# Kernel optimization log

Hardware: AMD Instinct MI355X
Metric: run time of the kernel (lower is better)

## Reference

```python
import jax, jax.numpy as jnp
import numpy as np

H, C = 4, 32            # num_heads, hidden_channels per head
HC = H * C
SLOPE_ATT = 0.2         # GATv2Conv negative_slope default
SLOPE_OUT = 0.01        # F.leaky_relu default

N_HOST, N_VM, N_JOB, N_SWITCH = 50000, 100000, 200000, 5000
IN_DIM = 64
E_HS, E_VH, E_JV = 200000, 400000, 800000


def _gatv2(x_src, x_dst, Wl, bl, Wr, br, att, bias, src, dst, n_dst):
    # PyG GATv2Conv (bipartite): lin_l on source, lin_r on destination
    xl = (x_src @ Wl + bl).reshape(-1, H, C)             # [Ns,H,C]
    xr = (x_dst @ Wr + br).reshape(-1, H, C)             # [Nd,H,C]
    e = jax.nn.leaky_relu(xl[src] + xr[dst], SLOPE_ATT)  # [E,H,C]
    logits = jnp.einsum('ehc,hc->eh', e, att)            # [E,H]
    m = jax.ops.segment_max(logits, dst, num_segments=n_dst)
    ex = jnp.exp(logits - m[dst])
    denom = jax.ops.segment_sum(ex, dst, num_segments=n_dst)
    alpha = ex / denom[dst]                              # scatter-softmax grouped by dst
    out = jax.ops.segment_sum(xl[src] * alpha[..., None], dst, num_segments=n_dst)
    return out.reshape(n_dst, HC) + bias, alpha


def setup_inputs() -> dict:
    key = jax.random.key(0)
    ks = iter(jax.random.split(key, 64))
    f32 = jnp.float32
    def randn(shape, scale=1.0):
        return jax.random.normal(next(ks), shape, dtype=f32) * scale
    sw = 1.0 / np.sqrt(IN_DIM)
    sa = 1.0 / np.sqrt(C)
    inp = {
        'x_host': randn((N_HOST, IN_DIM)),
        'x_vm': randn((N_VM, IN_DIM)),
        'x_job': randn((N_JOB, IN_DIM)),
        'x_switch': randn((N_SWITCH, IN_DIM)),
        'e_hs_src': jax.random.randint(next(ks), (E_HS,), 0, N_HOST),
        'e_hs_dst': jax.random.randint(next(ks), (E_HS,), 0, N_SWITCH),
        'e_vh_src': jax.random.randint(next(ks), (E_VH,), 0, N_VM),
        'e_vh_dst': jax.random.randint(next(ks), (E_VH,), 0, N_HOST),
        'e_jv_src': jax.random.randint(next(ks), (E_JV,), 0, N_JOB),
        'e_jv_dst': jax.random.randint(next(ks), (E_JV,), 0, N_VM),
    }
    for rel in ('hs', 'vh', 'jv'):
        inp['Wl_' + rel] = randn((IN_DIM, HC), sw)
        inp['bl_' + rel] = jnp.zeros((HC,), f32)
        inp['Wr_' + rel] = randn((IN_DIM, HC), sw)
        inp['br_' + rel] = jnp.zeros((HC,), f32)
        inp['att_' + rel] = randn((H, C), sa)
        inp['bias_' + rel] = jnp.zeros((HC,), f32)
    for nt in ('host', 'vm', 'job', 'switch'):
        inp['W_' + nt] = randn((HC, 1), 1.0 / np.sqrt(HC))
        inp['b_' + nt] = jnp.zeros((1,), f32)
    return inp


def reference(x_host, x_vm, x_job, x_switch,
              e_hs_src, e_hs_dst, e_vh_src, e_vh_dst, e_jv_src, e_jv_dst,
              Wl_hs, bl_hs, Wr_hs, br_hs, att_hs, bias_hs,
              Wl_vh, bl_vh, Wr_vh, br_vh, att_vh, bias_vh,
              Wl_jv, bl_jv, Wr_jv, br_jv, att_jv, bias_jv,
              W_host, b_host, W_vm, b_vm, W_job, b_job, W_switch, b_switch):
    out_switch, a_hs = _gatv2(x_host, x_switch, Wl_hs, bl_hs, Wr_hs, br_hs,
                              att_hs, bias_hs, e_hs_src, e_hs_dst, x_switch.shape[0])
    out_host, a_vh = _gatv2(x_vm, x_host, Wl_vh, bl_vh, Wr_vh, br_vh,
                            att_vh, bias_vh, e_vh_src, e_vh_dst, x_host.shape[0])
    out_vm, a_jv = _gatv2(x_job, x_vm, Wl_jv, bl_jv, Wr_jv, br_jv,
                          att_jv, bias_jv, e_jv_src, e_jv_dst, x_vm.shape[0])
    # each dst type receives exactly one relation; stack+sum is identity here
    h_host = jax.nn.leaky_relu(out_host, SLOPE_OUT)
    h_vm = jax.nn.leaky_relu(out_vm, SLOPE_OUT)
    h_switch = jax.nn.leaky_relu(out_switch, SLOPE_OUT)
    h_job = jnp.zeros((x_job.shape[0], HC), x_job.dtype)  # job has no incoming edges
    s_host = jax.nn.sigmoid(h_host @ W_host + b_host)
    s_vm = jax.nn.sigmoid(h_vm @ W_vm + b_vm)
    s_job = jax.nn.sigmoid(h_job @ W_job + b_job)
    s_switch = jax.nn.sigmoid(h_switch @ W_switch + b_switch)
    scores = jnp.concatenate([s_host, s_vm, s_job, s_switch], axis=0)
    return scores, a_hs, a_vh, a_jv
```

## Files before the change

kernel.cpp:

```cpp
#include <hip/hip_runtime.h>
#include <hip/hip_fp16.h>


#define SLOPE_ATT 0.2f
#define SLOPE_OUT 0.01f

typedef _Float16 half8_t __attribute__((ext_vector_type(8)));
typedef _Float16 v2h_t __attribute__((ext_vector_type(2)));
typedef float float4_t __attribute__((ext_vector_type(4)));

__device__ __forceinline__ float dot8(half8_t a, half8_t b, float acc) {
    v2h_t a0 = __builtin_shufflevector(a, a, 0, 1);
    v2h_t a1 = __builtin_shufflevector(a, a, 2, 3);
    v2h_t a2 = __builtin_shufflevector(a, a, 4, 5);
    v2h_t a3 = __builtin_shufflevector(a, a, 6, 7);
    v2h_t b0 = __builtin_shufflevector(b, b, 0, 1);
    v2h_t b1 = __builtin_shufflevector(b, b, 2, 3);
    v2h_t b2 = __builtin_shufflevector(b, b, 4, 5);
    v2h_t b3 = __builtin_shufflevector(b, b, 6, 7);
    acc = __builtin_amdgcn_fdot2(a0, b0, acc, false);
    acc = __builtin_amdgcn_fdot2(a1, b1, acc, false);
    acc = __builtin_amdgcn_fdot2(a2, b2, acc, false);
    acc = __builtin_amdgcn_fdot2(a3, b3, acc, false);
    return acc;
}

struct WSrc { const float* W[6]; };

__global__ __launch_bounds__(256) void init_wt_kernel(
    int* __restrict__ head, int ptot, WSrc wsrc, __half* __restrict__ Wt) {
    int i = blockIdx.x * 256 + threadIdx.x;
    if (i < ptot) {
        head[i] = -1;
    } else {
        int r = i - ptot;
        if (r < 6 * 8192) {
            int j = r >> 13;
            int rr = r & 8191;
            int n = rr >> 6, k = rr & 63;
            Wt[r] = (__half)wsrc.W[j][k * 128 + n];
        }
    }
}

__device__ __forceinline__ void link_work(
    int linkId, int linkBlocks,
    const int* __restrict__ d0, const int* __restrict__ s0,
    const int* __restrict__ d1, const int* __restrict__ s1,
    const int* __restrict__ d2, const int* __restrict__ s2,
    int* __restrict__ head, int2* __restrict__ nxt,
    int E0, int E1, int E2, int pb1, int pb2) {
    int i = linkId * 256 + threadIdx.x;
    int Etot = E0 + E1 + E2;
    int stride = linkBlocks * 256;
    for (; i < Etot; i += stride) {
        int le, slot; const int* sp;
        if (i < E0)           { le = i;           slot = d0[le];       sp = s0; }
        else if (i < E0 + E1) { le = i - E0;      slot = pb1 + d1[le]; sp = s1; }
        else                  { le = i - E0 - E1; slot = pb2 + d2[le]; sp = s2; }
        int old = atomicExch(&head[slot], le);
        nxt[i] = make_int2(old, sp[le]);
    }
}

struct GemmJobs {
    const float* X[6]; const float* b[6]; __half* Y[6];
    int M[6]; int pbase[7];
};

__global__ __launch_bounds__(256) void mega_gemm_link_kernel(
    GemmJobs j, const __half* __restrict__ Wt, int LB,
    const int* __restrict__ d0, const int* __restrict__ s0,
    const int* __restrict__ d1, const int* __restrict__ s1,
    const int* __restrict__ d2, const int* __restrict__ s2,
    int* __restrict__ head, int2* __restrict__ nxt,
    int E0, int E1, int E2, int pb1, int pb2) {
    __shared__ __half sY[4][16][136];
    int b = blockIdx.x;
    if (b < LB) {
        link_work(b, LB, d0, s0, d1, s1, d2, s2, head, nxt, E0, E1, E2, pb1, pb2);
        return;
    }
    int bb = b - LB;
    int k = 0;
    while (bb >= j.pbase[k + 1]) k++;
    const int p = bb - j.pbase[k];
    const int gb = j.pbase[k + 1] - j.pbase[k];
    const int M = j.M[k];
    const int nb = (M + 63) >> 6;
    if (p >= nb) return;
    const float* __restrict__ X = j.X[k];
    __half* __restrict__ Y = j.Y[k];
    const float* __restrict__ bb_ = j.b[k];
    const __half* __restrict__ W = Wt + (size_t)k * 8192;

    const int lane = threadIdx.x & 63;
    const int wv = threadIdx.x >> 6;
    const int mr = lane & 15;
    const int quad = lane >> 4;

    half8_t wb0[8], wb1[8];
    float bv[8];
#pragma unroll
    for (int t = 0; t < 8; t++) {
        const __half* wp = W + ((size_t)(t * 16 + mr)) * 64 + quad * 8;
        wb0[t] = *(const half8_t*)wp;
        wb1[t] = *(const half8_t*)(wp + 32);
        bv[t] = bb_[t * 16 + mr];
    }

    float4 xc0 = {}, xc1 = {}, xc2 = {}, xc3 = {};
    {
        int gr = p * 64 + wv * 16 + mr;
        if (gr < M) {
            const float4* xp = (const float4*)(X + (size_t)gr * 64 + quad * 8);
            xc0 = xp[0]; xc1 = xp[1];
            const float4* xq = (const float4*)(X + (size_t)gr * 64 + 32 + quad * 8);
            xc2 = xq[0]; xc3 = xq[1];
        }
    }

    for (int t = p; t < nb; t += gb) {
        int tn = t + gb;
        float4 xn0 = {}, xn1 = {}, xn2 = {}, xn3 = {};
        if (tn < nb) {
            int gr = tn * 64 + wv * 16 + mr;
            if (gr < M) {
                const float4* xp = (const float4*)(X + (size_t)gr * 64 + quad * 8);
                xn0 = xp[0]; xn1 = xp[1];
                const float4* xq = (const float4*)(X + (size_t)gr * 64 + 32 + quad * 8);
                xn2 = xq[0]; xn3 = xq[1];
            }
        }

        half8_t a0, a1;
        a0[0] = (_Float16)xc0.x; a0[1] = (_Float16)xc0.y;
        a0[2] = (_Float16)xc0.z; a0[3] = (_Float16)xc0.w;
        a0[4] = (_Float16)xc1.x; a0[5] = (_Float16)xc1.y;
        a0[6] = (_Float16)xc1.z; a0[7] = (_Float16)xc1.w;
        a1[0] = (_Float16)xc2.x; a1[1] = (_Float16)xc2.y;
        a1[2] = (_Float16)xc2.z; a1[3] = (_Float16)xc2.w;
        a1[4] = (_Float16)xc3.x; a1[5] = (_Float16)xc3.y;
        a1[6] = (_Float16)xc3.z; a1[7] = (_Float16)xc3.w;

        const int m0 = t * 64 + wv * 16;
#pragma unroll
        for (int tt = 0; tt < 8; tt++) {
            float4_t c = {0.f, 0.f, 0.f, 0.f};
            c = __builtin_amdgcn_mfma_f32_16x16x32_f16(a0, wb0[tt], c, 0, 0, 0);
            c = __builtin_amdgcn_mfma_f32_16x16x32_f16(a1, wb1[tt], c, 0, 0, 0);
            int ocol = tt * 16 + mr;
            int lrow = quad * 4;
#pragma unroll
            for (int r = 0; r < 4; r++)
                sY[wv][lrow + r][ocol] = (__half)(c[r] + bv[tt]);
        }

        const int c8 = mr * 8;
#pragma unroll
        for (int i = 0; i < 4; i++) {
            int row = i * 4 + quad;
            int gr2 = m0 + row;
            if (gr2 < M) {
                half8_t v = *(const half8_t*)&sY[wv][row][c8];
                *(half8_t*)&Y[(size_t)gr2 * 128 + c8] = v;
            }
        }

        xc0 = xn0; xc1 = xn1; xc2 = xn2; xc3 = xn3;
    }
}

struct AggJob {
    const __half* xl; const __half* xr; const float* att;
    const int* head; const int2* nxt;
    float* ex; float* dn;
    const float* bias; const float* Wn; const float* bn; float* scores;
    int Nd;
};
struct AggJobs { AggJob r[3]; int base[4]; };

__global__ __launch_bounds__(256) void agg3_kernel(AggJobs aj) {
    int b = blockIdx.x;
    int k = 0;
    while (b >= aj.base[k + 1]) k++;
    AggJob J = aj.r[k];

    const int l = threadIdx.x & 63;
    const int wv = threadIdx.x >> 6;
    const int li = l & 7;
    const int g = l >> 3;
    const int dbase = ((b - aj.base[k]) * 4 + wv) * 8;
    const int d = dbase + g;
    if (dbase >= J.Nd) return;
    const bool dok = d < J.Nd;
    const int h = li >> 1;

    half8_t xr0 = {}, xr1 = {};
    if (dok) {
        const half8_t* xrp = (const half8_t*)(J.xr + (size_t)d * 128) + li * 2;
        xr0 = xrp[0]; xr1 = xrp[1];
    }
    half8_t at0, at1;
    {
        const float* ap = J.att + li * 16;
#pragma unroll
        for (int i = 0; i < 8; i++) {
            at0[i] = (_Float16)ap[i];
            at1[i] = (_Float16)ap[8 + i];
        }
    }
    const half8_t sl8 = {(_Float16)SLOPE_ATT, (_Float16)SLOPE_ATT,
                         (_Float16)SLOPE_ATT, (_Float16)SLOPE_ATT,
                         (_Float16)SLOPE_ATT, (_Float16)SLOPE_ATT,
                         (_Float16)SLOPE_ATT, (_Float16)SLOPE_ATT};

    float acc[16] = {};
    float ssum = 0.f;

    int e = dok ? J.head[d] : -1;
    const bool any = (e >= 0);

    while (__any(e >= 0)) {
        bool act = (e >= 0);
        int2 ns = act ? J.nxt[e] : make_int2(-1, 0);
        half8_t x0 = {}, x1 = {};
        if (act) {
            const half8_t* xp = (const half8_t*)(J.xl + (size_t)ns.y * 128) + li * 2;
            x0 = xp[0]; x1 = xp[1];
        }
        if (act) {
            half8_t v0 = x0 + xr0;
            half8_t v1 = x1 + xr1;
            half8_t lk0 = __builtin_elementwise_max(v0, v0 * sl8);
            half8_t lk1 = __builtin_elementwise_max(v1, v1 * sl8);
            float p = dot8(lk1, at1, dot8(lk0, at0, 0.f));
            p += __shfl_xor(p, 1);
            float w = __expf(p);
            if ((li & 1) == 0) J.ex[(size_t)e * 4 + h] = w;
            ssum += w;
#pragma unroll
            for (int i = 0; i < 8; i++) {
                acc[i]     += w * (float)x0[i];
                acc[8 + i] += w * (float)x1[i];
            }
        }
        e = act ? ns.x : -1;
    }

    if (dok && (li & 1) == 0) J.dn[(size_t)d * 4 + h] = ssum;

    float rr = any ? 1.f / ssum : 0.f;
    float pr = 0.f;
    if (dok) {
        const float* bp = J.bias + li * 16;
        const float* wp = J.Wn + li * 16;
#pragma unroll
        for (int i = 0; i < 16; i++) {
            float o = acc[i] * rr + bp[i];
            o = o > 0.f ? o : SLOPE_OUT * o;
            pr += o * wp[i];
        }
    }
    pr += __shfl_xor(pr, 1);
    pr += __shfl_xor(pr, 2);
    pr += __shfl_xor(pr, 4);
    if (dok && li == 0)
        J.scores[d] = 1.f / (1.f + __expf(-(pr + J.bn[0])));
}

__global__ __launch_bounds__(256) void alpha_job_kernel(
    float* __restrict__ ex,
    const int* __restrict__ d0, const int* __restrict__ d1,
    const int* __restrict__ d2,
    const float* __restrict__ dn,
    int E0, int E1, int E2, int pb1, int pb2, int ab,
    const float* __restrict__ bjob, float* __restrict__ sjob, int NJ) {
    int b = blockIdx.x;
    if (b < ab) {
        int i = b * 256 + threadIdx.x;
        int tot = (E0 + E1 + E2) * 4;
        if (i >= tot) return;
        int e = i >> 2, h = i & 3;
        int d;
        if (e < E0)           d = d0[e];
        else if (e < E0 + E1) d = pb1 + d1[e - E0];
        else                  d = pb2 + d2[e - E0 - E1];
        ex[i] = ex[i] / dn[(size_t)d * 4 + h];
    } else {
        int i = (b - ab) * 256 + threadIdx.x;
        if (i < NJ) sjob[i] = 1.f / (1.f + __expf(-bjob[0]));
    }
}


extern "C" void kernel_launch(void* const* d_in, const int* in_sizes, int n_in,
                              void* d_out, int out_size, void* d_ws, size_t ws_size,
                              hipStream_t stream) {
    const float* x_host   = (const float*)d_in[0];
    const float* x_vm     = (const float*)d_in[1];
    const float* x_job    = (const float*)d_in[2];
    const float* x_switch = (const float*)d_in[3];
    const int* e_hs_src = (const int*)d_in[4];
    const int* e_hs_dst = (const int*)d_in[5];
    const int* e_vh_src = (const int*)d_in[6];
    const int* e_vh_dst = (const int*)d_in[7];
    const int* e_jv_src = (const int*)d_in[8];
    const int* e_jv_dst = (const int*)d_in[9];
    const float* Wl_hs = (const float*)d_in[10];
    const float* bl_hs = (const float*)d_in[11];
    const float* Wr_hs = (const float*)d_in[12];
    const float* br_hs = (const float*)d_in[13];
    const float* att_hs = (const float*)d_in[14];
    const float* bias_hs = (const float*)d_in[15];
    const float* Wl_vh = (const float*)d_in[16];
    const float* bl_vh = (const float*)d_in[17];
    const float* Wr_vh = (const float*)d_in[18];
    const float* br_vh = (const float*)d_in[19];
    const float* att_vh = (const float*)d_in[20];
    const float* bias_vh = (const float*)d_in[21];
    const float* Wl_jv = (const float*)d_in[22];
    const float* bl_jv = (const float*)d_in[23];
    const float* Wr_jv = (const float*)d_in[24];
    const float* br_jv = (const float*)d_in[25];
    const float* att_jv = (const float*)d_in[26];
    const float* bias_jv = (const float*)d_in[27];
    const float* W_host   = (const float*)d_in[28];
    const float* b_host   = (const float*)d_in[29];
    const float* W_vm     = (const float*)d_in[30];
    const float* b_vm     = (const float*)d_in[31];
    const float* W_job    = (const float*)d_in[32];
    const float* b_job    = (const float*)d_in[33];
    const float* W_switch = (const float*)d_in[34];
    const float* b_switch = (const float*)d_in[35];

    const int NH  = in_sizes[0] / 64;
    const int NV  = in_sizes[1] / 64;
    const int NJ  = in_sizes[2] / 64;
    const int NSW = in_sizes[3] / 64;
    const int EHS = in_sizes[4];
    const int EVH = in_sizes[6];
    const int EJV = in_sizes[8];
    const int Etot = EHS + EVH + EJV;

    float* out = (float*)d_out;
    float* s_host = out;
    float* s_vm = out + NH;
    float* s_job = out + NH + NV;
    float* s_sw = out + NH + NV + NJ;
    float* a_hs = out + NH + NV + NJ + NSW;
    float* a_vh = a_hs + (size_t)EHS * 4;
    float* a_jv = a_vh + (size_t)EVH * 4;

    const int pb1 = ((NSW + 255) / 256) * 256;
    const int pb2 = pb1 + ((NH + 255) / 256) * 256;
    const int ptot = pb2 + ((NV + 255) / 256) * 256;

    float* ws = (float*)d_ws;
    int2* nxt_all = (int2*)ws;
    int* head_all = (int*)(nxt_all + Etot);
    float* dn_all = (float*)(head_all + ptot);
    __half* Wt    = (__half*)(dn_all + (size_t)ptot * 4);
    __half* mats  = Wt + 6 * 8192;
    __half* xl_hs = mats;
    __half* xr_hs = xl_hs + (size_t)NH * 128;
    __half* xl_vh = xr_hs + (size_t)NSW * 128;
    __half* xr_vh = xl_vh + (size_t)NV * 128;
    __half* xl_jv = xr_vh + (size_t)NH * 128;
    __half* xr_jv = xl_jv + (size_t)NJ * 128;

    {
        WSrc w;
        w.W[0] = Wl_hs; w.W[1] = Wr_hs; w.W[2] = Wl_vh;
        w.W[3] = Wr_vh; w.W[4] = Wl_jv; w.W[5] = Wr_jv;
        int tot = ptot + 6 * 8192;
        init_wt_kernel<<<(tot + 255) / 256, 256, 0, stream>>>(head_all, ptot, w, Wt);
    }

    {
        GemmJobs j;
        const float* Xs[6] = {x_host, x_switch, x_vm, x_host, x_job, x_vm};
        const float* bs[6] = {bl_hs, br_hs, bl_vh, br_vh, bl_jv, br_jv};
        __half* Ys[6] = {xl_hs, xr_hs, xl_vh, xr_vh, xl_jv, xr_jv};
        int Ms[6] = {NH, NSW, NV, NH, NJ, NV};
        int nbk[6]; long long total_nb = 0;
        for (int k = 0; k < 6; k++) { nbk[k] = (Ms[k] + 63) / 64; total_nb += nbk[k]; }
        const int GBTOT = 1664;
        const int LB = 384;
        int pb = 0;
        for (int k = 0; k < 6; k++) {
            j.X[k] = Xs[k]; j.b[k] = bs[k]; j.Y[k] = Ys[k]; j.M[k] = Ms[k];
            j.pbase[k] = pb;
            int gb = (int)(((long long)GBTOT * nbk[k]) / total_nb);
            if (gb < 1) gb = 1;
            pb += gb;
        }
        j.pbase[6] = pb;
        mega_gemm_link_kernel<<<LB + pb, 256, 0, stream>>>(
            j, Wt, LB, e_hs_dst, e_hs_src, e_vh_dst, e_vh_src,
            e_jv_dst, e_jv_src, head_all, nxt_all, EHS, EVH, EJV, pb1, pb2);
    }

    {
        AggJobs aj;
        aj.r[0] = {xl_hs, xr_hs, att_hs, head_all + 0, nxt_all + 0,
                   a_hs, dn_all + 0,
                   bias_hs, W_switch, b_switch, s_sw, NSW};
        aj.r[1] = {xl_vh, xr_vh, att_vh, head_all + pb1, nxt_all + EHS,
                   a_vh, dn_all + (size_t)pb1 * 4,
                   bias_vh, W_host, b_host, s_host, NH};
        aj.r[2] = {xl_jv, xr_jv, att_jv, head_all + pb2, nxt_all + (EHS + EVH),
                   a_jv, dn_all + (size_t)pb2 * 4,
                   bias_jv, W_vm, b_vm, s_vm, NV};
        aj.base[0] = 0;
        aj.base[1] = (NSW + 31) / 32;
        aj.base[2] = aj.base[1] + (NH + 31) / 32;
        aj.base[3] = aj.base[2] + (NV + 31) / 32;
        agg3_kernel<<<aj.base[3], 256, 0, stream>>>(aj);
    }

    {
        int ab = (Etot * 4 + 255) / 256;
        int jb = (NJ + 255) / 256;
        alpha_job_kernel<<<ab + jb, 256, 0, stream>>>(
            a_hs, e_hs_dst, e_vh_dst, e_jv_dst, dn_all,
            EHS, EVH, EJV, pb1, pb2, ab, b_job, s_job, NJ);
    }
}
```

Before: 367.5 us.

## Fuse alpha normalization into aggregation kernel via second linked-list walk

Drops the separate alpha_job_kernel. After computing the softmax denominator, each destination group walks its edge linked list again and rescales the stored exp values in place, so the dn buffer and the gather of dst indices go away. The job-score sigmoid fill moves into the init kernel, and the aggregation kernel shrinks to 128-thread blocks to get more, smaller blocks. This costs a second pointer-chasing pass over each adjacency list, whose nxt and ex accesses are dependent and likely uncached, in exchange for removing one launch and a full pass over the edges.

```diff
diff --git a/kernel.cpp b/kernel.cpp
--- a/kernel.cpp
+++ b/kernel.cpp
@@ -28,7 +28,8 @@
 struct WSrc { const float* W[6]; };
 
 __global__ __launch_bounds__(256) void init_wt_kernel(
-    int* __restrict__ head, int ptot, WSrc wsrc, __half* __restrict__ Wt) {
+    int* __restrict__ head, int ptot, WSrc wsrc, __half* __restrict__ Wt,
+    const float* __restrict__ bjob, float* __restrict__ sjob, int NJ) {
     int i = blockIdx.x * 256 + threadIdx.x;
     if (i < ptot) {
         head[i] = -1;
@@ -39,6 +40,9 @@
             int rr = r & 8191;
             int n = rr >> 6, k = rr & 63;
             Wt[r] = (__half)wsrc.W[j][k * 128 + n];
+        } else {
+            int q = r - 6 * 8192;
+            if (q < NJ) sjob[q] = 1.f / (1.f + __expf(-bjob[0]));
         }
     }
 }
@@ -174,13 +178,13 @@
 struct AggJob {
     const __half* xl; const __half* xr; const float* att;
     const int* head; const int2* nxt;
-    float* ex; float* dn;
+    float* ex;
     const float* bias; const float* Wn; const float* bn; float* scores;
     int Nd;
 };
 struct AggJobs { AggJob r[3]; int base[4]; };
 
-__global__ __launch_bounds__(256) void agg3_kernel(AggJobs aj) {
+__global__ __launch_bounds__(128) void agg3_kernel(AggJobs aj) {
     int b = blockIdx.x;
     int k = 0;
     while (b >= aj.base[k + 1]) k++;
@@ -190,7 +194,7 @@
     const int wv = threadIdx.x >> 6;
     const int li = l & 7;
     const int g = l >> 3;
-    const int dbase = ((b - aj.base[k]) * 4 + wv) * 8;
+    const int dbase = ((b - aj.base[k]) * 2 + wv) * 8;
     const int d = dbase + g;
     if (dbase >= J.Nd) return;
     const bool dok = d < J.Nd;
@@ -248,8 +252,6 @@
         e = act ? ns.x : -1;
     }
 
-    if (dok && (li & 1) == 0) J.dn[(size_t)d * 4 + h] = ssum;
-
     float rr = any ? 1.f / ssum : 0.f;
     float pr = 0.f;
     if (dok) {
@@ -267,29 +269,16 @@
     pr += __shfl_xor(pr, 4);
     if (dok && li == 0)
         J.scores[d] = 1.f / (1.f + __expf(-(pr + J.bn[0])));
-}
-
-__global__ __launch_bounds__(256) void alpha_job_kernel(
-    float* __restrict__ ex,
-    const int* __restrict__ d0, const int* __restrict__ d1,
-    const int* __restrict__ d2,
-    const float* __restrict__ dn,
-    int E0, int E1, int E2, int pb1, int pb2, int ab,
-    const float* __restrict__ bjob, float* __restrict__ sjob, int NJ) {
-    int b = blockIdx.x;
-    if (b < ab) {
-        int i = b * 256 + threadIdx.x;
-        int tot = (E0 + E1 + E2) * 4;
-        if (i >= tot) return;
-        int e = i >> 2, h = i & 3;
-        int d;
-        if (e < E0)           d = d0[e];
-        else if (e < E0 + E1) d = pb1 + d1[e - E0];
-        else                  d = pb2 + d2[e - E0 - E1];
-        ex[i] = ex[i] / dn[(size_t)d * 4 + h];
-    } else {
-        int i = (b - ab) * 256 + threadIdx.x;
-        if (i < NJ) sjob[i] = 1.f / (1.f + __expf(-bjob[0]));
+
+    int e2 = dok ? J.head[d] : -1;
+    while (__any(e2 >= 0)) {
+        bool act = (e2 >= 0);
+        int2 ns = act ? J.nxt[e2] : make_int2(-1, 0);
+        if (act && (li & 1) == 0) {
+            size_t o = (size_t)e2 * 4 + h;
+            J.ex[o] = J.ex[o] * rr;
+        }
+        e2 = act ? ns.x : -1;
     }
 }
 
@@ -373,8 +362,9 @@
         WSrc w;
         w.W[0] = Wl_hs; w.W[1] = Wr_hs; w.W[2] = Wl_vh;
         w.W[3] = Wr_vh; w.W[4] = Wl_jv; w.W[5] = Wr_jv;
-        int tot = ptot + 6 * 8192;
-        init_wt_kernel<<<(tot + 255) / 256, 256, 0, stream>>>(head_all, ptot, w, Wt);
+        int tot = ptot + 6 * 8192 + NJ;
+        init_wt_kernel<<<(tot + 255) / 256, 256, 0, stream>>>(
+            head_all, ptot, w, Wt, b_job, s_job, NJ);
     }
 
     {
@@ -404,26 +394,15 @@
     {
         AggJobs aj;
         aj.r[0] = {xl_hs, xr_hs, att_hs, head_all + 0, nxt_all + 0,
-                   a_hs, dn_all + 0,
-                   bias_hs, W_switch, b_switch, s_sw, NSW};
+                   a_hs, bias_hs, W_switch, b_switch, s_sw, NSW};
         aj.r[1] = {xl_vh, xr_vh, att_vh, head_all + pb1, nxt_all + EHS,
-                   a_vh, dn_all + (size_t)pb1 * 4,
-                   bias_vh, W_host, b_host, s_host, NH};
+                   a_vh, bias_vh, W_host, b_host, s_host, NH};
         aj.r[2] = {xl_jv, xr_jv, att_jv, head_all + pb2, nxt_all + (EHS + EVH),
-                   a_jv, dn_all + (size_t)pb2 * 4,
-                   bias_jv, W_vm, b_vm, s_vm, NV};
+                   a_jv, bias_jv, W_vm, b_vm, s_vm, NV};
         aj.base[0] = 0;
-        aj.base[1] = (NSW + 31) / 32;
-        aj.base[2] = aj.base[1] + (NH + 31) / 32;
-        aj.base[3] = aj.base[2] + (NV + 31) / 32;
-        agg3_kernel<<<aj.base[3], 256, 0, stream>>>(aj);
-    }
-
-    {
-        int ab = (Etot * 4 + 255) / 256;
-        int jb = (NJ + 255) / 256;
-        alpha_job_kernel<<<ab + jb, 256, 0, stream>>>(
-            a_hs, e_hs_dst, e_vh_dst, e_jv_dst, dn_all,
-            EHS, EVH, EJV, pb1, pb2, ab, b_job, s_job, NJ);
-    }
-}
+        aj.base[1] = (NSW + 15) / 16;
+        aj.base[2] = aj.base[1] + (NH + 15) / 16;
+        aj.base[3] = aj.base[2] + (NV + 15) / 16;
+        agg3_kernel<<<aj.base[3], 128, 0, stream>>>(aj);
+    }
+}
```

After: 406.6 us. +10.7%, slower.

## Schedule GEMM tiles dynamically via atomic ticket and shrink aggregation blocks

Applied to the files above, without the earlier changes.

Replaces the static per-matrix block partition of the fused GEMM/link kernel with a persistent grid that grabs chunks of 16-row tiles through an atomic ticket counter. Weights are reloaded only when a chunk crosses into a different matrix, and the link-building blocks also join the GEMM pool after they finish their edge work. The job-score sigmoid fill and ticket reset move into the init kernel, and aggregation blocks shrink from 256 to 128 threads. The aim is better load balance and less tail idle time, at the cost of atomic contention and smaller per-wave tiles.

```diff
diff --git a/kernel.cpp b/kernel.cpp
--- a/kernel.cpp
+++ b/kernel.cpp
@@ -4,6 +4,7 @@
 
 #define SLOPE_ATT 0.2f
 #define SLOPE_OUT 0.01f
+#define CHUNK 8
 
 typedef _Float16 half8_t __attribute__((ext_vector_type(8)));
 typedef _Float16 v2h_t __attribute__((ext_vector_type(2)));
@@ -28,7 +29,9 @@
 struct WSrc { const float* W[6]; };
 
 __global__ __launch_bounds__(256) void init_wt_kernel(
-    int* __restrict__ head, int ptot, WSrc wsrc, __half* __restrict__ Wt) {
+    int* __restrict__ head, int ptot, WSrc wsrc, __half* __restrict__ Wt,
+    const float* __restrict__ bjob, float* __restrict__ sjob, int NJ,
+    int* __restrict__ ticket) {
     int i = blockIdx.x * 256 + threadIdx.x;
     if (i < ptot) {
         head[i] = -1;
@@ -39,6 +42,10 @@
             int rr = r & 8191;
             int n = rr >> 6, k = rr & 63;
             Wt[r] = (__half)wsrc.W[j][k * 128 + n];
+        } else {
+            int q = r - 6 * 8192;
+            if (q < NJ) sjob[q] = 1.f / (1.f + __expf(-bjob[0]));
+            else if (q - NJ < 8) ticket[q - NJ] = 0;
         }
     }
 }
@@ -65,11 +72,12 @@
 
 struct GemmJobs {
     const float* X[6]; const float* b[6]; __half* Y[6];
-    int M[6]; int pbase[7];
+    int M[6]; int sbase[7];
 };
 
 __global__ __launch_bounds__(256) void mega_gemm_link_kernel(
-    GemmJobs j, const __half* __restrict__ Wt, int LB,
+    GemmJobs j, const __half* __restrict__ Wt, int* __restrict__ ticket,
+    int LB,
     const int* __restrict__ d0, const int* __restrict__ s0,
     const int* __restrict__ d1, const int* __restrict__ s1,
     const int* __restrict__ d2, const int* __restrict__ s2,
@@ -77,97 +85,108 @@
     int E0, int E1, int E2, int pb1, int pb2) {
     __shared__ __half sY[4][16][136];
     int b = blockIdx.x;
-    if (b < LB) {
+    if (b < LB)
         link_work(b, LB, d0, s0, d1, s1, d2, s2, head, nxt, E0, E1, E2, pb1, pb2);
-        return;
-    }
-    int bb = b - LB;
-    int k = 0;
-    while (bb >= j.pbase[k + 1]) k++;
-    const int p = bb - j.pbase[k];
-    const int gb = j.pbase[k + 1] - j.pbase[k];
-    const int M = j.M[k];
-    const int nb = (M + 63) >> 6;
-    if (p >= nb) return;
-    const float* __restrict__ X = j.X[k];
-    __half* __restrict__ Y = j.Y[k];
-    const float* __restrict__ bb_ = j.b[k];
-    const __half* __restrict__ W = Wt + (size_t)k * 8192;
 
     const int lane = threadIdx.x & 63;
     const int wv = threadIdx.x >> 6;
     const int mr = lane & 15;
     const int quad = lane >> 4;
-
+    const int nbtot = j.sbase[6];
+
+    int kc = -1;
     half8_t wb0[8], wb1[8];
     float bv[8];
-#pragma unroll
-    for (int t = 0; t < 8; t++) {
-        const __half* wp = W + ((size_t)(t * 16 + mr)) * 64 + quad * 8;
-        wb0[t] = *(const half8_t*)wp;
-        wb1[t] = *(const half8_t*)(wp + 32);
-        bv[t] = bb_[t * 16 + mr];
-    }
-
-    float4 xc0 = {}, xc1 = {}, xc2 = {}, xc3 = {};
-    {
-        int gr = p * 64 + wv * 16 + mr;
-        if (gr < M) {
-            const float4* xp = (const float4*)(X + (size_t)gr * 64 + quad * 8);
-            xc0 = xp[0]; xc1 = xp[1];
-            const float4* xq = (const float4*)(X + (size_t)gr * 64 + 32 + quad * 8);
-            xc2 = xq[0]; xc3 = xq[1];
-        }
-    }
-
-    for (int t = p; t < nb; t += gb) {
-        int tn = t + gb;
-        float4 xn0 = {}, xn1 = {}, xn2 = {}, xn3 = {};
-        if (tn < nb) {
-            int gr = tn * 64 + wv * 16 + mr;
-            if (gr < M) {
+
+    for (;;) {
+        int c = 0;
+        if (lane == 0) c = atomicAdd(ticket, 1);
+        c = __shfl(c, 0);
+        int g0 = c * CHUNK;
+        if (g0 >= nbtot) break;
+        int g1 = g0 + CHUNK; if (g1 > nbtot) g1 = nbtot;
+
+        int k = 0;
+        while (g0 >= j.sbase[k + 1]) k++;
+        float4 xc0 = {}, xc1 = {}, xc2 = {}, xc3 = {};
+        {
+            int gr = (g0 - j.sbase[k]) * 16 + mr;
+            if (gr < j.M[k]) {
+                const float* X = j.X[k];
                 const float4* xp = (const float4*)(X + (size_t)gr * 64 + quad * 8);
-                xn0 = xp[0]; xn1 = xp[1];
+                xc0 = xp[0]; xc1 = xp[1];
                 const float4* xq = (const float4*)(X + (size_t)gr * 64 + 32 + quad * 8);
-                xn2 = xq[0]; xn3 = xq[1];
-            }
-        }
-
-        half8_t a0, a1;
-        a0[0] = (_Float16)xc0.x; a0[1] = (_Float16)xc0.y;
-        a0[2] = (_Float16)xc0.z; a0[3] = (_Float16)xc0.w;
-        a0[4] = (_Float16)xc1.x; a0[5] = (_Float16)xc1.y;
-        a0[6] = (_Float16)xc1.z; a0[7] = (_Float16)xc1.w;
-        a1[0] = (_Float16)xc2.x; a1[1] = (_Float16)xc2.y;
-        a1[2] = (_Float16)xc2.z; a1[3] = (_Float16)xc2.w;
-        a1[4] = (_Float16)xc3.x; a1[5] = (_Float16)xc3.y;
-        a1[6] = (_Float16)xc3.z; a1[7] = (_Float16)xc3.w;
-
-        const int m0 = t * 64 + wv * 16;
-#pragma unroll
-        for (int tt = 0; tt < 8; tt++) {
-            float4_t c = {0.f, 0.f, 0.f, 0.f};
-            c = __builtin_amdgcn_mfma_f32_16x16x32_f16(a0, wb0[tt], c, 0, 0, 0);
-            c = __builtin_amdgcn_mfma_f32_16x16x32_f16(a1, wb1[tt], c, 0, 0, 0);
-            int ocol = tt * 16 + mr;
-            int lrow = quad * 4;
-#pragma unroll
-            for (int r = 0; r < 4; r++)
-                sY[wv][lrow + r][ocol] = (__half)(c[r] + bv[tt]);
-        }
-
-        const int c8 = mr * 8;
-#pragma unroll
-        for (int i = 0; i < 4; i++) {
-            int row = i * 4 + quad;
-            int gr2 = m0 + row;
-            if (gr2 < M) {
-                half8_t v = *(const half8_t*)&sY[wv][row][c8];
-                *(half8_t*)&Y[(size_t)gr2 * 128 + c8] = v;
-            }
-        }
-
-        xc0 = xn0; xc1 = xn1; xc2 = xn2; xc3 = xn3;
+                xc2 = xq[0]; xc3 = xq[1];
+            }
+        }
+
+        for (int g = g0; g < g1; ++g) {
+            float4 xn0 = {}, xn1 = {}, xn2 = {}, xn3 = {};
+            int kn = k;
+            if (g + 1 < g1) {
+                while (g + 1 >= j.sbase[kn + 1]) kn++;
+                int gr = (g + 1 - j.sbase[kn]) * 16 + mr;
+                if (gr < j.M[kn]) {
+                    const float* X = j.X[kn];
+                    const float4* xp = (const float4*)(X + (size_t)gr * 64 + quad * 8);
+                    xn0 = xp[0]; xn1 = xp[1];
+                    const float4* xq = (const float4*)(X + (size_t)gr * 64 + 32 + quad * 8);
+                    xn2 = xq[0]; xn3 = xq[1];
+                }
+            }
+
+            if (k != kc) {
+                kc = k;
+                const __half* W = Wt + (size_t)k * 8192;
+                const float* bb_ = j.b[k];
+#pragma unroll
+                for (int t = 0; t < 8; t++) {
+                    const __half* wp = W + ((size_t)(t * 16 + mr)) * 64 + quad * 8;
+                    wb0[t] = *(const half8_t*)wp;
+                    wb1[t] = *(const half8_t*)(wp + 32);
+                    bv[t] = bb_[t * 16 + mr];
+                }
+            }
+
+            half8_t a0, a1;
+            a0[0] = (_Float16)xc0.x; a0[1] = (_Float16)xc0.y;
+            a0[2] = (_Float16)xc0.z; a0[3] = (_Float16)xc0.w;
+            a0[4] = (_Float16)xc1.x; a0[5] = (_Float16)xc1.y;
+            a0[6] = (_Float16)xc1.z; a0[7] = (_Float16)xc1.w;
+            a1[0] = (_Float16)xc2.x; a1[1] = (_Float16)xc2.y;
+            a1[2] = (_Float16)xc2.z; a1[3] = (_Float16)xc2.w;
+            a1[4] = (_Float16)xc3.x; a1[5] = (_Float16)xc3.y;
+            a1[6] = (_Float16)xc3.z; a1[7] = (_Float16)xc3.w;
+
+            const int M = j.M[k];
+            __half* __restrict__ Y = j.Y[k];
+            const int m0 = (g - j.sbase[k]) * 16;
+#pragma unroll
+            for (int tt = 0; tt < 8; tt++) {
+                float4_t creg = {0.f, 0.f, 0.f, 0.f};
+                creg = __builtin_amdgcn_mfma_f32_16x16x32_f16(a0, wb0[tt], creg, 0, 0, 0);
+                creg = __builtin_amdgcn_mfma_f32_16x16x32_f16(a1, wb1[tt], creg, 0, 0, 0);
+                int ocol = tt * 16 + mr;
+                int lrow = quad * 4;
+#pragma unroll
+                for (int r = 0; r < 4; r++)
+                    sY[wv][lrow + r][ocol] = (__half)(creg[r] + bv[tt]);
+            }
+
+            const int c8 = mr * 8;
+#pragma unroll
+            for (int i = 0; i < 4; i++) {
+                int row = i * 4 + quad;
+                int gr2 = m0 + row;
+                if (gr2 < M) {
+                    half8_t v = *(const half8_t*)&sY[wv][row][c8];
+                    *(half8_t*)&Y[(size_t)gr2 * 128 + c8] = v;
+                }
+            }
+
+            xc0 = xn0; xc1 = xn1; xc2 = xn2; xc3 = xn3;
+            k = kn;
+        }
     }
 }
 
@@ -180,7 +199,7 @@
 };
 struct AggJobs { AggJob r[3]; int base[4]; };
 
-__global__ __launch_bounds__(256) void agg3_kernel(AggJobs aj) {
+__global__ __launch_bounds__(128) void agg3_kernel(AggJobs aj) {
     int b = blockIdx.x;
     int k = 0;
     while (b >= aj.base[k + 1]) k++;
@@ -190,7 +209,7 @@
     const int wv = threadIdx.x >> 6;
     const int li = l & 7;
     const int g = l >> 3;
-    const int dbase = ((b - aj.base[k]) * 4 + wv) * 8;
+    const int dbase = ((b - aj.base[k]) * 2 + wv) * 8;
     const int d = dbase + g;
     if (dbase >= J.Nd) return;
     const bool dok = d < J.Nd;
@@ -269,28 +288,21 @@
         J.scores[d] = 1.f / (1.f + __expf(-(pr + J.bn[0])));
 }
 
-__global__ __launch_bounds__(256) void alpha_job_kernel(
+__global__ __launch_bounds__(256) void alpha_kernel(
     float* __restrict__ ex,
     const int* __restrict__ d0, const int* __restrict__ d1,
     const int* __restrict__ d2,
     const float* __restrict__ dn,
-    int E0, int E1, int E2, int pb1, int pb2, int ab,
-    const float* __restrict__ bjob, float* __restrict__ sjob, int NJ) {
-    int b = blockIdx.x;
-    if (b < ab) {
-        int i = b * 256 + threadIdx.x;
-        int tot = (E0 + E1 + E2) * 4;
-        if (i >= tot) return;
-        int e = i >> 2, h = i & 3;
-        int d;
-        if (e < E0)           d = d0[e];
-        else if (e < E0 + E1) d = pb1 + d1[e - E0];
-        else                  d = pb2 + d2[e - E0 - E1];
-        ex[i] = ex[i] / dn[(size_t)d * 4 + h];
-    } else {
-        int i = (b - ab) * 256 + threadIdx.x;
-        if (i < NJ) sjob[i] = 1.f / (1.f + __expf(-bjob[0]));
-    }
+    int E0, int E1, int E2, int pb1, int pb2) {
+    int i = blockIdx.x * 256 + threadIdx.x;
+    int tot = (E0 + E1 + E2) * 4;
+    if (i >= tot) return;
+    int e = i >> 2, h = i & 3;
+    int d;
+    if (e < E0)           d = d0[e];
+    else if (e < E0 + E1) d = pb1 + d1[e - E0];
+    else                  d = pb2 + d2[e - E0 - E1];
+    ex[i] = ex[i] / dn[(size_t)d * 4 + h];
 }
 
 
@@ -360,7 +372,8 @@
     int2* nxt_all = (int2*)ws;
     int* head_all = (int*)(nxt_all + Etot);
     float* dn_all = (float*)(head_all + ptot);
-    __half* Wt    = (__half*)(dn_all + (size_t)ptot * 4);
+    int* ticket   = (int*)(dn_all + (size_t)ptot * 4);
+    __half* Wt    = (__half*)(ticket + 8);
     __half* mats  = Wt + 6 * 8192;
     __half* xl_hs = mats;
     __half* xr_hs = xl_hs + (size_t)NH * 128;
@@ -373,8 +386,9 @@
         WSrc w;
         w.W[0] = Wl_hs; w.W[1] = Wr_hs; w.W[2] = Wl_vh;
         w.W[3] = Wr_vh; w.W[4] = Wl_jv; w.W[5] = Wr_jv;
-        int tot = ptot + 6 * 8192;
-        init_wt_kernel<<<(tot + 255) / 256, 256, 0, stream>>>(head_all, ptot, w, Wt);
+        int tot = ptot + 6 * 8192 + NJ + 8;
+        init_wt_kernel<<<(tot + 255) / 256, 256, 0, stream>>>(
+            head_all, ptot, w, Wt, b_job, s_job, NJ, ticket);
     }
 
     {
@@ -383,21 +397,17 @@
         const float* bs[6] = {bl_hs, br_hs, bl_vh, br_vh, bl_jv, br_jv};
         __half* Ys[6] = {xl_hs, xr_hs, xl_vh, xr_vh, xl_jv, xr_jv};
         int Ms[6] = {NH, NSW, NV, NH, NJ, NV};
-        int nbk[6]; long long total_nb = 0;
-        for (int k = 0; k < 6; k++) { nbk[k] = (Ms[k] + 63) / 64; total_nb += nbk[k]; }
-        const int GBTOT = 1664;
-        const int LB = 384;
-        int pb = 0;
+        int sb = 0;
         for (int k = 0; k < 6; k++) {
             j.X[k] = Xs[k]; j.b[k] = bs[k]; j.Y[k] = Ys[k]; j.M[k] = Ms[k];
-            j.pbase[k] = pb;
-            int gb = (int)(((long long)GBTOT * nbk[k]) / total_nb);
-            if (gb < 1) gb = 1;
-            pb += gb;
-        }
-        j.pbase[6] = pb;
-        mega_gemm_link_kernel<<<LB + pb, 256, 0, stream>>>(
-            j, Wt, LB, e_hs_dst, e_hs_src, e_vh_dst, e_vh_src,
+            j.sbase[k] = sb;
+            sb += (Ms[k] + 15) / 16;
+        }
+        j.sbase[6] = sb;
+        const int LB = 384;
+        const int T = 2048;
+        mega_gemm_link_kernel<<<T, 256, 0, stream>>>(
+            j, Wt, ticket, LB, e_hs_dst, e_hs_src, e_vh_dst, e_vh_src,
             e_jv_dst, e_jv_src, head_all, nxt_all, EHS, EVH, EJV, pb1, pb2);
     }
 
@@ -413,17 +423,16 @@
                    a_jv, dn_all + (size_t)pb2 * 4,
                    bias_jv, W_vm, b_vm, s_vm, NV};
         aj.base[0] = 0;
-        aj.base[1] = (NSW + 31) / 32;
-        aj.base[2] = aj.base[1] + (NH + 31) / 32;
-        aj.base[3] = aj.base[2] + (NV + 31) / 32;
-        agg3_kernel<<<aj.base[3], 256, 0, stream>>>(aj);
+        aj.base[1] = (NSW + 15) / 16;
+        aj.base[2] = aj.base[1] + (NH + 15) / 16;
+        aj.base[3] = aj.base[2] + (NV + 15) / 16;
+        agg3_kernel<<<aj.base[3], 128, 0, stream>>>(aj);
     }
 
     {
         int ab = (Etot * 4 + 255) / 256;
-        int jb = (NJ + 255) / 256;
-        alpha_job_kernel<<<ab + jb, 256, 0, stream>>>(
+        alpha_kernel<<<ab, 256, 0, stream>>>(
             a_hs, e_hs_dst, e_vh_dst, e_jv_dst, dn_all,
-            EHS, EVH, EJV, pb1, pb2, ab, b_job, s_job, NJ);
-    }
-}
+            EHS, EVH, EJV, pb1, pb2);
+    }
+}
```

After: 489.8 us. 33.3% more time.
